# Optimization experiments

Measured on AMD Instinct MI355X. Metric: run time of the kernel, lower is better.

Reference implementation:

```python
import jax, jax.numpy as jnp
import numpy as np

TOPK = 2
ALPHA = 32.0
EPS = 1e-20


def setup_inputs() -> dict:
    key = jax.random.key(0)
    ks = jax.random.split(key, 6)
    E, D, R, Q, V = 16, 2048, 16, 2048, 512
    B, S = 2, 2048
    return {
        "hidden_states": jax.random.normal(ks[0], (B, S, D), jnp.float32),
        "router_weight": jax.random.normal(ks[1], (E, D), jnp.float32) * 0.02,
        "q_lora_a": jax.random.normal(ks[2], (E, D, R), jnp.float32) * 0.02,
        "q_lora_b": jax.random.normal(ks[3], (E, R, Q), jnp.float32) * 0.02,
        "v_lora_a": jax.random.normal(ks[4], (E, D, R), jnp.float32) * 0.02,
        "v_lora_b": jax.random.normal(ks[5], (E, R, V), jnp.float32) * 0.02,
    }


def reference(hidden_states, router_weight, q_lora_a, q_lora_b, v_lora_a, v_lora_b):
    E, D, R = q_lora_a.shape
    Qo = q_lora_b.shape[-1]
    Vo = v_lora_b.shape[-1]
    scale = ALPHA / float(R)
    orig_shape = hidden_states.shape[:-1]
    h = hidden_states.reshape(-1, D)  # [n, D]
    n = h.shape[0]

    # router: top-k softmax probs, renormalized over the k selected experts
    logits = jnp.einsum('nd,ed->ne', h, router_weight)
    probs = jax.nn.softmax(logits, axis=-1)
    scores, idx = jax.lax.top_k(probs, TOPK)          # [n, k]
    scores = scores / (scores.sum(-1, keepdims=True) + EPS)

    # per-token expert combine weights c[n, e] = scale * sum_k score_k * 1[idx_k == e]
    c = jnp.zeros((n, E), h.dtype).at[jnp.arange(n)[:, None], idx].add(scores * scale)

    # dense per-expert low-rank projections; weighting by c makes non-selected
    # experts contribute zero -> identical math to gather + einsum + weighted sum.
    q_low = jnp.einsum('nd,edr->ner', h, q_lora_a) * c[..., None]  # [n, E, R]
    v_low = jnp.einsum('nd,edr->ner', h, v_lora_a) * c[..., None]
    q_delta = jnp.einsum('ner,erq->nq', q_low, q_lora_b)
    v_delta = jnp.einsum('ner,erv->nv', v_low, v_lora_b)

    return (q_delta.reshape(*orig_shape, Qo), v_delta.reshape(*orig_shape, Vo))
```

## Files before the change

### kernel.cpp

```cpp
#include <hip/hip_runtime.h>
#include <math.h>

#define DD 2048
#define EE 16
#define RR 16
#define QO 2048
#define VO 512
#define TILE 128
#define BATCH 16
#define DSPLIT 4
#define DRANGE (DD / DSPLIT)
#define DC 64
#define HSTR (DC + 4)
#define ASTR 20
#define RDC 256
#define T2 32
#define CGQ (QO / 256)
#define CGV (VO / 256)

struct Route { int i0, i1; float w0, w1; };

__global__ __launch_bounds__(256) void router_kernel(
    const float* __restrict__ h, const float* __restrict__ rw,
    Route* __restrict__ route, int n)
{
    __shared__ float  hs[8 * RDC];
    __shared__ double slogd[8 * EE];

    int t0 = blockIdx.x * 8;
    int e  = threadIdx.x >> 4;
    int l  = threadIdx.x & 15;

    double acc[8];
#pragma unroll
    for (int t = 0; t < 8; ++t) acc[t] = 0.0;

    for (int d0 = 0; d0 < DD; d0 += RDC) {
        __syncthreads();
        for (int i = threadIdx.x; i < 8 * (RDC / 4); i += 256) {
            int t = i >> 6, dq = (i & 63) * 4;
            float4 v = make_float4(0.f, 0.f, 0.f, 0.f);
            if (t0 + t < n)
                v = *(const float4*)&h[(size_t)(t0 + t) * DD + d0 + dq];
            *(float4*)&hs[t * RDC + dq] = v;
        }
        __syncthreads();
        const float* rwe = rw + e * DD + d0;
#pragma unroll
        for (int g = 0; g < RDC / 64; ++g) {
            int d = g * 64 + l * 4;
            float4 r4 = *(const float4*)&rwe[d];
            double rx = r4.x, ry = r4.y, rz = r4.z, rw4 = r4.w;
#pragma unroll
            for (int t = 0; t < 8; ++t) {
                float4 hv = *(const float4*)&hs[t * RDC + d];
                acc[t] += (double)hv.x * rx + (double)hv.y * ry
                        + (double)hv.z * rz + (double)hv.w * rw4;
            }
        }
    }
#pragma unroll
    for (int t = 0; t < 8; ++t) {
#pragma unroll
        for (int off = 8; off; off >>= 1)
            acc[t] += __shfl_down(acc[t], off, 16);
    }
    if (l == 0) {
#pragma unroll
        for (int t = 0; t < 8; ++t) slogd[t * EE + e] = acc[t];
    }
    __syncthreads();

    if (threadIdx.x < 8) {
        int t = threadIdx.x, tok = t0 + t;
        if (tok < n) {
            double lg[EE];
#pragma unroll
            for (int i = 0; i < EE; ++i) lg[i] = slogd[t * EE + i];
            int i0 = 0;
            for (int i = 1; i < EE; ++i) if (lg[i] > lg[i0]) i0 = i;
            int i1 = -1;
            for (int i = 0; i < EE; ++i)
                if (i != i0 && (i1 < 0 || lg[i] > lg[i1])) i1 = i;
            double mx = lg[i0], Z = 0.0;
            for (int i = 0; i < EE; ++i) Z += exp(lg[i] - mx);
            double p0 = 1.0 / Z;
            double p1 = exp(lg[i1] - mx) / Z;
            double s  = p0 + p1 + 1e-20;
            Route rt;
            rt.i0 = i0; rt.i1 = i1;
            rt.w0 = (float)(2.0 * p0 / s);
            rt.w1 = (float)(2.0 * p1 / s);
            route[tok] = rt;
        }
    }
}

__global__ __launch_bounds__(256) void a_kernel(
    const float* __restrict__ h, const Route* __restrict__ route,
    const float* __restrict__ qa, const float* __restrict__ va,
    float* __restrict__ low, int n)
{
    int e  = blockIdx.x;
    int t0 = blockIdx.y * TILE;
    int ds = blockIdx.z;

    __shared__ int   sel_tok[TILE];
    __shared__ float sel_w[TILE];
    __shared__ int   sel_k[TILE];
    __shared__ int   sm_cnt;
    if (threadIdx.x == 0) sm_cnt = 0;
    __syncthreads();
    for (int i = threadIdx.x; i < TILE; i += 256) {
        int tok = t0 + i;
        if (tok < n) {
            Route rt = route[tok];
            float w = 0.f; int sel = 0, k = 0;
            if      (rt.i0 == e) { sel = 1; w = rt.w0; k = 0; }
            else if (rt.i1 == e) { sel = 1; w = rt.w1; k = 1; }
            if (sel) {
                int p = atomicAdd(&sm_cnt, 1);
                sel_tok[p] = tok; sel_w[p] = w; sel_k[p] = k;
            }
        }
    }
    __syncthreads();
    int m = sm_cnt;
    if (m == 0) return;

    __align__(16) __shared__ float aq_s[DC * ASTR];
    __align__(16) __shared__ float av_s[DC * ASTR];
    __align__(16) __shared__ float hs[BATCH * HSTR];

    const float* qa_e = qa + (size_t)e * DD * RR;
    const float* va_e = va + (size_t)e * DD * RR;

    int s    = threadIdx.x & 15;
    int tile = threadIdx.x >> 4;
    int tp   = tile >> 2;
    int rp   = tile & 3;

    for (int b0 = 0; b0 < m; b0 += BATCH) {
        int mb = min(BATCH, m - b0);

        float accq[4][4], accv[4][4];
#pragma unroll
        for (int ti = 0; ti < 4; ++ti)
#pragma unroll
            for (int ri = 0; ri < 4; ++ri) { accq[ti][ri] = 0.f; accv[ti][ri] = 0.f; }

        for (int d0 = ds * DRANGE; d0 < (ds + 1) * DRANGE; d0 += DC) {
            __syncthreads();
            {
                int i = threadIdx.x;
                int d = i >> 2, rf = (i & 3) * 4;
                *(float4*)&aq_s[d * ASTR + rf] = *(const float4*)&qa_e[(size_t)(d0 + d) * RR + rf];
                *(float4*)&av_s[d * ASTR + rf] = *(const float4*)&va_e[(size_t)(d0 + d) * RR + rf];
            }
            {
                int i = threadIdx.x;
                int j = i >> 4, dq = (i & 15) * 4;
                float4 v = make_float4(0.f, 0.f, 0.f, 0.f);
                if (j < mb)
                    v = *(const float4*)&h[(size_t)sel_tok[b0 + j] * DD + d0 + dq];
                *(float4*)&hs[j * HSTR + dq] = v;
            }
            __syncthreads();
#pragma unroll
            for (int dd = 0; dd < DC / 16; ++dd) {
                int d = (dd << 4) + s;
                float hv[4];
#pragma unroll
                for (int ti = 0; ti < 4; ++ti)
                    hv[ti] = hs[(tp * 4 + ti) * HSTR + d];
                float4 aqv = *(const float4*)&aq_s[d * ASTR + rp * 4];
                float4 avv = *(const float4*)&av_s[d * ASTR + rp * 4];
                const float* aqp = &aqv.x;
                const float* avp = &avv.x;
#pragma unroll
                for (int ti = 0; ti < 4; ++ti)
#pragma unroll
                    for (int ri = 0; ri < 4; ++ri) {
                        accq[ti][ri] = fmaf(hv[ti], aqp[ri], accq[ti][ri]);
                        accv[ti][ri] = fmaf(hv[ti], avp[ri], accv[ti][ri]);
                    }
            }
        }
#pragma unroll
        for (int ti = 0; ti < 4; ++ti)
#pragma unroll
            for (int ri = 0; ri < 4; ++ri) {
#pragma unroll
                for (int off = 8; off; off >>= 1) {
                    accq[ti][ri] += __shfl_down(accq[ti][ri], off, 16);
                    accv[ti][ri] += __shfl_down(accv[ti][ri], off, 16);
                }
            }
        if (s == 0) {
#pragma unroll
            for (int ti = 0; ti < 4; ++ti) {
                int t = tp * 4 + ti;
                if (t < mb) {
                    int   tok = sel_tok[b0 + t];
                    int   k   = sel_k[b0 + t];
                    float w   = sel_w[b0 + t];
                    size_t base = ((size_t)(tok * 2 + k) * DSPLIT + ds) * 32;
#pragma unroll
                    for (int ri = 0; ri < 4; ++ri) {
                        low[base + rp * 4 + ri]      = accq[ti][ri] * w;
                        low[base + 16 + rp * 4 + ri] = accv[ti][ri] * w;
                    }
                }
            }
        }
        __syncthreads();
    }
}

__global__ __launch_bounds__(256) void b_kernel(
    const Route* __restrict__ route, const float* __restrict__ low,
    const float* __restrict__ qb, const float* __restrict__ vb,
    float* __restrict__ outq, float* __restrict__ outv, int n)
{
    int t0 = blockIdx.x * T2;
    int cg = blockIdx.y;
    int tid = threadIdx.x;

    __shared__ float acc_s[T2 * 256];
    __shared__ float ls[T2 * 2 * RR];
    __shared__ int   elist[EE * T2];
    __shared__ int   ecnt[EE];
    __shared__ Route rts[T2];

    if (tid < EE) ecnt[tid] = 0;
    if (tid < T2) {
        int tok = t0 + tid;
        if (tok < n) rts[tid] = route[tok];
        else { rts[tid].i0 = -1; rts[tid].i1 = -1; rts[tid].w0 = 0.f; rts[tid].w1 = 0.f; }
    }
    __syncthreads();
    if (tid < T2 * 2) {
        int j = tid >> 1, k = tid & 1;
        int e = k ? rts[j].i1 : rts[j].i0;
        if (e >= 0) {
            int p = atomicAdd(&ecnt[e], 1);
            elist[e * T2 + p] = j * 2 + k;
        }
    }
    int side = (cg >= CGQ) ? 1 : 0;
    {
        int slot = tid >> 2, r4 = (tid & 3) * 4;
        int j = slot >> 1, k = slot & 1;
        int tok = t0 + j;
        float4 v = make_float4(0.f, 0.f, 0.f, 0.f);
        if (tok < n) {
            const float* lp = low + (size_t)(tok * 2 + k) * (DSPLIT * 32) + side * 16 + r4;
            float4 p0 = *(const float4*)(lp);
            float4 p1 = *(const float4*)(lp + 32);
            float4 p2 = *(const float4*)(lp + 64);
            float4 p3 = *(const float4*)(lp + 96);
            v.x = p0.x + p1.x + p2.x + p3.x;
            v.y = p0.y + p1.y + p2.y + p3.y;
            v.z = p0.z + p1.z + p2.z + p3.z;
            v.w = p0.w + p1.w + p2.w + p3.w;
        }
        *(float4*)&ls[slot * RR + r4] = v;
    }
#pragma unroll
    for (int j = 0; j < T2; ++j) acc_s[j * 256 + tid] = 0.f;
    __syncthreads();

    const float* bp; float* outp; int W, colbase;
    if (cg < CGQ) { bp = qb; outp = outq; W = QO; colbase = cg * 256; }
    else          { bp = vb; outp = outv; W = VO; colbase = (cg - CGQ) * 256; }
    int col = colbase + tid;

    for (int e = 0; e < EE; ++e) {
        int c = ecnt[e];
        if (c == 0) continue;
        const float* be = bp + (size_t)e * RR * W + col;
        float bc[RR];
#pragma unroll
        for (int r = 0; r < RR; ++r) bc[r] = be[(size_t)r * W];
        for (int ii = 0; ii < c; ++ii) {
            int sk = elist[e * T2 + ii];
            int j  = sk >> 1;
            const float* lp = &ls[sk * RR];
            float4 l0 = *(const float4*)(lp);
            float4 l1 = *(const float4*)(lp + 4);
            float4 l2 = *(const float4*)(lp + 8);
            float4 l3 = *(const float4*)(lp + 12);
            float v = 0.f;
            v = fmaf(l0.x, bc[0],  v); v = fmaf(l0.y, bc[1],  v);
            v = fmaf(l0.z, bc[2],  v); v = fmaf(l0.w, bc[3],  v);
            v = fmaf(l1.x, bc[4],  v); v = fmaf(l1.y, bc[5],  v);
            v = fmaf(l1.z, bc[6],  v); v = fmaf(l1.w, bc[7],  v);
            v = fmaf(l2.x, bc[8],  v); v = fmaf(l2.y, bc[9],  v);
            v = fmaf(l2.z, bc[10], v); v = fmaf(l2.w, bc[11], v);
            v = fmaf(l3.x, bc[12], v); v = fmaf(l3.y, bc[13], v);
            v = fmaf(l3.z, bc[14], v); v = fmaf(l3.w, bc[15], v);
            acc_s[j * 256 + tid] += v;
        }
    }
#pragma unroll
    for (int j = 0; j < T2; ++j) {
        int tok = t0 + j;
        if (tok < n) outp[(size_t)tok * W + col] = acc_s[j * 256 + tid];
    }
}

extern "C" void kernel_launch(void* const* d_in, const int* in_sizes, int n_in,
                              void* d_out, int out_size, void* d_ws, size_t ws_size,
                              hipStream_t stream) {
    const float* h  = (const float*)d_in[0];
    const float* rw = (const float*)d_in[1];
    const float* qa = (const float*)d_in[2];
    const float* qb = (const float*)d_in[3];
    const float* va = (const float*)d_in[4];
    const float* vb = (const float*)d_in[5];

    int n = in_sizes[0] / DD;
    float* out  = (float*)d_out;
    float* outq = out;
    float* outv = out + (size_t)n * QO;

    Route* route = (Route*)d_ws;
    float* low   = (float*)((char*)d_ws + (((size_t)n * 16 + 255) & ~(size_t)255));

    int tiles = (n + TILE - 1) / TILE;

    router_kernel<<<(n + 7) / 8, 256, 0, stream>>>(h, rw, route, n);

    dim3 g2(EE, tiles, DSPLIT);
    a_kernel<<<g2, 256, 0, stream>>>(h, route, qa, va, low, n);

    dim3 g3((n + T2 - 1) / T2, CGQ + CGV);
    b_kernel<<<g3, 256, 0, stream>>>(route, low, qb, vb, outq, outv, n);
}
```

Before: 221.9 us.

## Restructure MoE LoRA kernels: whole-slice A staging, finer D split, prefetched B

The router kernel now handles 4 tokens per block instead of 8, which doubles the number of blocks. The A kernel now stages each expert's whole D-slice of the LoRA A matrices in shared memory once and reuses it across token batches. It splits D eight ways when the workspace is large enough, otherwise four ways with q and v done in two passes. The B kernel builds a compact list of active experts, prefetches the next expert's B columns into registers, and writes outputs as vectorized float4 stores from shared memory. These changes aim to cut repeated A-matrix loads and raise parallelism, at the cost of more shared memory per block, lower occupancy, and more partial sums for the B kernel to reduce.

```diff
diff --git a/kernel.cpp b/kernel.cpp
--- a/kernel.cpp
+++ b/kernel.cpp
@@ -8,15 +8,11 @@
 #define VO 512
 #define TILE 128
 #define BATCH 16
-#define DSPLIT 4
-#define DRANGE (DD / DSPLIT)
-#define DC 64
-#define HSTR (DC + 4)
-#define ASTR 20
+#define T2 32
+#define CGQ 8
+#define CGV 2
+#define RTB 4
 #define RDC 256
-#define T2 32
-#define CGQ (QO / 256)
-#define CGV (VO / 256)
 
 struct Route { int i0, i1; float w0, w1; };
 
@@ -24,21 +20,19 @@
     const float* __restrict__ h, const float* __restrict__ rw,
     Route* __restrict__ route, int n)
 {
-    __shared__ float  hs[8 * RDC];
-    __shared__ double slogd[8 * EE];
-
-    int t0 = blockIdx.x * 8;
+    __shared__ float  hs[RTB * RDC];
+    __shared__ double slogd[RTB * EE];
+
+    int t0 = blockIdx.x * RTB;
     int e  = threadIdx.x >> 4;
     int l  = threadIdx.x & 15;
 
-    double acc[8];
-#pragma unroll
-    for (int t = 0; t < 8; ++t) acc[t] = 0.0;
+    double acc[RTB] = {0.0, 0.0, 0.0, 0.0};
 
     for (int d0 = 0; d0 < DD; d0 += RDC) {
         __syncthreads();
-        for (int i = threadIdx.x; i < 8 * (RDC / 4); i += 256) {
-            int t = i >> 6, dq = (i & 63) * 4;
+        {
+            int t = threadIdx.x >> 6, dq = (threadIdx.x & 63) * 4;
             float4 v = make_float4(0.f, 0.f, 0.f, 0.f);
             if (t0 + t < n)
                 v = *(const float4*)&h[(size_t)(t0 + t) * DD + d0 + dq];
@@ -52,7 +46,7 @@
             float4 r4 = *(const float4*)&rwe[d];
             double rx = r4.x, ry = r4.y, rz = r4.z, rw4 = r4.w;
 #pragma unroll
-            for (int t = 0; t < 8; ++t) {
+            for (int t = 0; t < RTB; ++t) {
                 float4 hv = *(const float4*)&hs[t * RDC + d];
                 acc[t] += (double)hv.x * rx + (double)hv.y * ry
                         + (double)hv.z * rz + (double)hv.w * rw4;
@@ -60,18 +54,18 @@
         }
     }
 #pragma unroll
-    for (int t = 0; t < 8; ++t) {
+    for (int t = 0; t < RTB; ++t) {
 #pragma unroll
         for (int off = 8; off; off >>= 1)
             acc[t] += __shfl_down(acc[t], off, 16);
     }
     if (l == 0) {
 #pragma unroll
-        for (int t = 0; t < 8; ++t) slogd[t * EE + e] = acc[t];
-    }
-    __syncthreads();
-
-    if (threadIdx.x < 8) {
+        for (int t = 0; t < RTB; ++t) slogd[t * EE + e] = acc[t];
+    }
+    __syncthreads();
+
+    if (threadIdx.x < RTB) {
         int t = threadIdx.x, tok = t0 + t;
         if (tok < n) {
             double lg[EE];
@@ -96,11 +90,13 @@
     }
 }
 
+template<int DSPLIT, bool TWOPASS>
 __global__ __launch_bounds__(256) void a_kernel(
     const float* __restrict__ h, const Route* __restrict__ route,
     const float* __restrict__ qa, const float* __restrict__ va,
     float* __restrict__ low, int n)
 {
+    constexpr int DR = DD / DSPLIT;
     int e  = blockIdx.x;
     int t0 = blockIdx.y * TILE;
     int ds = blockIdx.z;
@@ -115,12 +111,12 @@
         int tok = t0 + i;
         if (tok < n) {
             Route rt = route[tok];
-            float w = 0.f; int sel = 0, k = 0;
-            if      (rt.i0 == e) { sel = 1; w = rt.w0; k = 0; }
-            else if (rt.i1 == e) { sel = 1; w = rt.w1; k = 1; }
-            if (sel) {
+            if (rt.i0 == e) {
                 int p = atomicAdd(&sm_cnt, 1);
-                sel_tok[p] = tok; sel_w[p] = w; sel_k[p] = k;
+                sel_tok[p] = tok; sel_w[p] = rt.w0; sel_k[p] = 0;
+            } else if (rt.i1 == e) {
+                int p = atomicAdd(&sm_cnt, 1);
+                sel_tok[p] = tok; sel_w[p] = rt.w1; sel_k[p] = 1;
             }
         }
     }
@@ -128,95 +124,145 @@
     int m = sm_cnt;
     if (m == 0) return;
 
-    __align__(16) __shared__ float aq_s[DC * ASTR];
-    __align__(16) __shared__ float av_s[DC * ASTR];
-    __align__(16) __shared__ float hs[BATCH * HSTR];
-
-    const float* qa_e = qa + (size_t)e * DD * RR;
-    const float* va_e = va + (size_t)e * DD * RR;
+    __align__(16) __shared__ float a_s[(TWOPASS ? 1 : 2) * DR * RR];
+    __align__(16) __shared__ float hs[BATCH * DR];
+
+    const float* aq_e = qa + (size_t)e * DD * RR + (size_t)ds * DR * RR;
+    const float* av_e = va + (size_t)e * DD * RR + (size_t)ds * DR * RR;
 
     int s    = threadIdx.x & 15;
     int tile = threadIdx.x >> 4;
     int tp   = tile >> 2;
     int rp   = tile & 3;
 
-    for (int b0 = 0; b0 < m; b0 += BATCH) {
-        int mb = min(BATCH, m - b0);
-
-        float accq[4][4], accv[4][4];
-#pragma unroll
-        for (int ti = 0; ti < 4; ++ti)
-#pragma unroll
-            for (int ri = 0; ri < 4; ++ri) { accq[ti][ri] = 0.f; accv[ti][ri] = 0.f; }
-
-        for (int d0 = ds * DRANGE; d0 < (ds + 1) * DRANGE; d0 += DC) {
+    constexpr int NMAT = TWOPASS ? 2 : 1;
+    for (int mat = 0; mat < NMAT; ++mat) {
+        __syncthreads();
+        if (TWOPASS) {
+            const float* ap = mat ? av_e : aq_e;
+            for (int t = threadIdx.x; t < DR * RR / 4; t += 256) {
+                int d = t >> 2, rf = (t & 3) * 4;
+                *(float4*)&a_s[d * RR + rf] = *(const float4*)&ap[(size_t)d * RR + rf];
+            }
+        } else {
+            for (int t = threadIdx.x; t < 2 * DR * RR / 4; t += 256) {
+                int which = t >= DR * RR / 4;
+                int tt = which ? t - DR * RR / 4 : t;
+                int d = tt >> 2, rf = (tt & 3) * 4;
+                const float* ap = which ? av_e : aq_e;
+                *(float4*)&a_s[which * DR * RR + d * RR + rf] =
+                    *(const float4*)&ap[(size_t)d * RR + rf];
+            }
+        }
+
+        for (int b0 = 0; b0 < m; b0 += BATCH) {
+            int mb = min(BATCH, m - b0);
             __syncthreads();
-            {
-                int i = threadIdx.x;
-                int d = i >> 2, rf = (i & 3) * 4;
-                *(float4*)&aq_s[d * ASTR + rf] = *(const float4*)&qa_e[(size_t)(d0 + d) * RR + rf];
-                *(float4*)&av_s[d * ASTR + rf] = *(const float4*)&va_e[(size_t)(d0 + d) * RR + rf];
-            }
-            {
-                int i = threadIdx.x;
-                int j = i >> 4, dq = (i & 15) * 4;
+            for (int t = threadIdx.x; t < BATCH * DR / 4; t += 256) {
+                int j = t / (DR / 4), f = (t % (DR / 4)) * 4;
                 float4 v = make_float4(0.f, 0.f, 0.f, 0.f);
                 if (j < mb)
-                    v = *(const float4*)&h[(size_t)sel_tok[b0 + j] * DD + d0 + dq];
-                *(float4*)&hs[j * HSTR + dq] = v;
+                    v = *(const float4*)&h[(size_t)sel_tok[b0 + j] * DD + ds * DR + f];
+                *(float4*)&hs[j * DR + f] = v;
             }
             __syncthreads();
-#pragma unroll
-            for (int dd = 0; dd < DC / 16; ++dd) {
-                int d = (dd << 4) + s;
-                float hv[4];
+
+            if (!TWOPASS) {
+                float accq[4][4] = {}, accv[4][4] = {};
+#pragma unroll
+                for (int dd = 0; dd < DR / 16; ++dd) {
+                    int d = dd * 16 + s;
+                    float4 a0 = *(const float4*)&a_s[d * RR + rp * 4];
+                    float4 a1 = *(const float4*)&a_s[DR * RR + d * RR + rp * 4];
+                    float hv[4];
+#pragma unroll
+                    for (int ti = 0; ti < 4; ++ti)
+                        hv[ti] = hs[(tp * 4 + ti) * DR + d];
+                    const float* q4 = &a0.x;
+                    const float* v4 = &a1.x;
+#pragma unroll
+                    for (int ti = 0; ti < 4; ++ti)
+#pragma unroll
+                        for (int ri = 0; ri < 4; ++ri) {
+                            accq[ti][ri] = fmaf(hv[ti], q4[ri], accq[ti][ri]);
+                            accv[ti][ri] = fmaf(hv[ti], v4[ri], accv[ti][ri]);
+                        }
+                }
 #pragma unroll
                 for (int ti = 0; ti < 4; ++ti)
-                    hv[ti] = hs[(tp * 4 + ti) * HSTR + d];
-                float4 aqv = *(const float4*)&aq_s[d * ASTR + rp * 4];
-                float4 avv = *(const float4*)&av_s[d * ASTR + rp * 4];
-                const float* aqp = &aqv.x;
-                const float* avp = &avv.x;
-#pragma unroll
-                for (int ti = 0; ti < 4; ++ti)
 #pragma unroll
                     for (int ri = 0; ri < 4; ++ri) {
-                        accq[ti][ri] = fmaf(hv[ti], aqp[ri], accq[ti][ri]);
-                        accv[ti][ri] = fmaf(hv[ti], avp[ri], accv[ti][ri]);
+#pragma unroll
+                        for (int off = 8; off; off >>= 1) {
+                            accq[ti][ri] += __shfl_down(accq[ti][ri], off, 16);
+                            accv[ti][ri] += __shfl_down(accv[ti][ri], off, 16);
+                        }
                     }
-            }
-        }
-#pragma unroll
-        for (int ti = 0; ti < 4; ++ti)
-#pragma unroll
-            for (int ri = 0; ri < 4; ++ri) {
-#pragma unroll
-                for (int off = 8; off; off >>= 1) {
-                    accq[ti][ri] += __shfl_down(accq[ti][ri], off, 16);
-                    accv[ti][ri] += __shfl_down(accv[ti][ri], off, 16);
-                }
-            }
-        if (s == 0) {
-#pragma unroll
-            for (int ti = 0; ti < 4; ++ti) {
-                int t = tp * 4 + ti;
-                if (t < mb) {
-                    int   tok = sel_tok[b0 + t];
-                    int   k   = sel_k[b0 + t];
-                    float w   = sel_w[b0 + t];
-                    size_t base = ((size_t)(tok * 2 + k) * DSPLIT + ds) * 32;
-#pragma unroll
-                    for (int ri = 0; ri < 4; ++ri) {
-                        low[base + rp * 4 + ri]      = accq[ti][ri] * w;
-                        low[base + 16 + rp * 4 + ri] = accv[ti][ri] * w;
+                if (s == 0) {
+#pragma unroll
+                    for (int ti = 0; ti < 4; ++ti) {
+                        int t = tp * 4 + ti;
+                        if (t < mb) {
+                            int   tok = sel_tok[b0 + t];
+                            int   k   = sel_k[b0 + t];
+                            float w   = sel_w[b0 + t];
+                            float* dst = low + ((size_t)(tok * 2 + k) * DSPLIT + ds) * 32;
+                            float4 vq = make_float4(accq[ti][0]*w, accq[ti][1]*w,
+                                                    accq[ti][2]*w, accq[ti][3]*w);
+                            float4 vv = make_float4(accv[ti][0]*w, accv[ti][1]*w,
+                                                    accv[ti][2]*w, accv[ti][3]*w);
+                            *(float4*)&dst[rp * 4]      = vq;
+                            *(float4*)&dst[16 + rp * 4] = vv;
+                        }
                     }
                 }
-            }
-        }
-        __syncthreads();
+            } else {
+                float acc[4][4] = {};
+#pragma unroll
+                for (int dd = 0; dd < DR / 16; ++dd) {
+                    int d = dd * 16 + s;
+                    float4 a0 = *(const float4*)&a_s[d * RR + rp * 4];
+                    float hv[4];
+#pragma unroll
+                    for (int ti = 0; ti < 4; ++ti)
+                        hv[ti] = hs[(tp * 4 + ti) * DR + d];
+                    const float* q4 = &a0.x;
+#pragma unroll
+                    for (int ti = 0; ti < 4; ++ti)
+#pragma unroll
+                        for (int ri = 0; ri < 4; ++ri)
+                            acc[ti][ri] = fmaf(hv[ti], q4[ri], acc[ti][ri]);
+                }
+#pragma unroll
+                for (int ti = 0; ti < 4; ++ti)
+#pragma unroll
+                    for (int ri = 0; ri < 4; ++ri) {
+#pragma unroll
+                        for (int off = 8; off; off >>= 1)
+                            acc[ti][ri] += __shfl_down(acc[ti][ri], off, 16);
+                    }
+                if (s == 0) {
+#pragma unroll
+                    for (int ti = 0; ti < 4; ++ti) {
+                        int t = tp * 4 + ti;
+                        if (t < mb) {
+                            int   tok = sel_tok[b0 + t];
+                            int   k   = sel_k[b0 + t];
+                            float w   = sel_w[b0 + t];
+                            float* dst = low + ((size_t)(tok * 2 + k) * DSPLIT + ds) * 32
+                                       + mat * 16;
+                            float4 vq = make_float4(acc[ti][0]*w, acc[ti][1]*w,
+                                                    acc[ti][2]*w, acc[ti][3]*w);
+                            *(float4*)&dst[rp * 4] = vq;
+                        }
+                    }
+                }
+            }
+        }
     }
 }
 
+template<int DSPLIT>
 __global__ __launch_bounds__(256) void b_kernel(
     const Route* __restrict__ route, const float* __restrict__ low,
     const float* __restrict__ qb, const float* __restrict__ vb,
@@ -230,13 +276,17 @@
     __shared__ float ls[T2 * 2 * RR];
     __shared__ int   elist[EE * T2];
     __shared__ int   ecnt[EE];
+    __shared__ int   plist[EE];
+    __shared__ int   pcnt;
     __shared__ Route rts[T2];
 
     if (tid < EE) ecnt[tid] = 0;
+    if (tid == 0) pcnt = 0;
     if (tid < T2) {
         int tok = t0 + tid;
-        if (tok < n) rts[tid] = route[tok];
-        else { rts[tid].i0 = -1; rts[tid].i1 = -1; rts[tid].w0 = 0.f; rts[tid].w1 = 0.f; }
+        Route rt; rt.i0 = -1; rt.i1 = -1; rt.w0 = 0.f; rt.w1 = 0.f;
+        if (tok < n) rt = route[tok];
+        rts[tid] = rt;
     }
     __syncthreads();
     if (tid < T2 * 2) {
@@ -250,62 +300,79 @@
     int side = (cg >= CGQ) ? 1 : 0;
     {
         int slot = tid >> 2, r4 = (tid & 3) * 4;
-        int j = slot >> 1, k = slot & 1;
-        int tok = t0 + j;
+        int j = slot >> 1;
         float4 v = make_float4(0.f, 0.f, 0.f, 0.f);
-        if (tok < n) {
-            const float* lp = low + (size_t)(tok * 2 + k) * (DSPLIT * 32) + side * 16 + r4;
-            float4 p0 = *(const float4*)(lp);
-            float4 p1 = *(const float4*)(lp + 32);
-            float4 p2 = *(const float4*)(lp + 64);
-            float4 p3 = *(const float4*)(lp + 96);
-            v.x = p0.x + p1.x + p2.x + p3.x;
-            v.y = p0.y + p1.y + p2.y + p3.y;
-            v.z = p0.z + p1.z + p2.z + p3.z;
-            v.w = p0.w + p1.w + p2.w + p3.w;
+        if (t0 + j < n) {
+            const float* lp = low + (size_t)((t0 + j) * 2 + (slot & 1)) * (DSPLIT * 32)
+                            + side * 16 + r4;
+#pragma unroll
+            for (int p = 0; p < DSPLIT; ++p) {
+                float4 q = *(const float4*)(lp + p * 32);
+                v.x += q.x; v.y += q.y; v.z += q.z; v.w += q.w;
+            }
         }
         *(float4*)&ls[slot * RR + r4] = v;
     }
 #pragma unroll
     for (int j = 0; j < T2; ++j) acc_s[j * 256 + tid] = 0.f;
     __syncthreads();
+    if (tid < EE && ecnt[tid] > 0) { int p = atomicAdd(&pcnt, 1); plist[p] = tid; }
+    __syncthreads();
+    int P = pcnt;
 
     const float* bp; float* outp; int W, colbase;
     if (cg < CGQ) { bp = qb; outp = outq; W = QO; colbase = cg * 256; }
     else          { bp = vb; outp = outv; W = VO; colbase = (cg - CGQ) * 256; }
     int col = colbase + tid;
 
-    for (int e = 0; e < EE; ++e) {
-        int c = ecnt[e];
-        if (c == 0) continue;
-        const float* be = bp + (size_t)e * RR * W + col;
+    if (P > 0) {
         float bc[RR];
-#pragma unroll
-        for (int r = 0; r < RR; ++r) bc[r] = be[(size_t)r * W];
-        for (int ii = 0; ii < c; ++ii) {
-            int sk = elist[e * T2 + ii];
-            int j  = sk >> 1;
-            const float* lp = &ls[sk * RR];
-            float4 l0 = *(const float4*)(lp);
-            float4 l1 = *(const float4*)(lp + 4);
-            float4 l2 = *(const float4*)(lp + 8);
-            float4 l3 = *(const float4*)(lp + 12);
-            float v = 0.f;
-            v = fmaf(l0.x, bc[0],  v); v = fmaf(l0.y, bc[1],  v);
-            v = fmaf(l0.z, bc[2],  v); v = fmaf(l0.w, bc[3],  v);
-            v = fmaf(l1.x, bc[4],  v); v = fmaf(l1.y, bc[5],  v);
-            v = fmaf(l1.z, bc[6],  v); v = fmaf(l1.w, bc[7],  v);
-            v = fmaf(l2.x, bc[8],  v); v = fmaf(l2.y, bc[9],  v);
-            v = fmaf(l2.z, bc[10], v); v = fmaf(l2.w, bc[11], v);
-            v = fmaf(l3.x, bc[12], v); v = fmaf(l3.y, bc[13], v);
-            v = fmaf(l3.z, bc[14], v); v = fmaf(l3.w, bc[15], v);
-            acc_s[j * 256 + tid] += v;
-        }
-    }
-#pragma unroll
-    for (int j = 0; j < T2; ++j) {
+        {
+            const float* be = bp + (size_t)plist[0] * RR * W + col;
+#pragma unroll
+            for (int r = 0; r < RR; ++r) bc[r] = be[(size_t)r * W];
+        }
+        for (int p = 0; p < P; ++p) {
+            float bn[RR];
+            if (p + 1 < P) {
+                const float* be = bp + (size_t)plist[p + 1] * RR * W + col;
+#pragma unroll
+                for (int r = 0; r < RR; ++r) bn[r] = be[(size_t)r * W];
+            }
+            int e = plist[p], c = ecnt[e];
+            for (int ii = 0; ii < c; ++ii) {
+                int sk = elist[e * T2 + ii];
+                int j  = sk >> 1;
+                const float* lp = &ls[sk * RR];
+                float4 l0 = *(const float4*)(lp);
+                float4 l1 = *(const float4*)(lp + 4);
+                float4 l2 = *(const float4*)(lp + 8);
+                float4 l3 = *(const float4*)(lp + 12);
+                float v = 0.f;
+                v = fmaf(l0.x, bc[0],  v); v = fmaf(l0.y, bc[1],  v);
+                v = fmaf(l0.z, bc[2],  v); v = fmaf(l0.w, bc[3],  v);
+                v = fmaf(l1.x, bc[4],  v); v = fmaf(l1.y, bc[5],  v);
+                v = fmaf(l1.z, bc[6],  v); v = fmaf(l1.w, bc[7],  v);
+                v = fmaf(l2.x, bc[8],  v); v = fmaf(l2.y, bc[9],  v);
+                v = fmaf(l2.z, bc[10], v); v = fmaf(l2.w, bc[11], v);
+                v = fmaf(l3.x, bc[12], v); v = fmaf(l3.y, bc[13], v);
+                v = fmaf(l3.z, bc[14], v); v = fmaf(l3.w, bc[15], v);
+                acc_s[j * 256 + tid] += v;
+            }
+            if (p + 1 < P) {
+#pragma unroll
+                for (int r = 0; r < RR; ++r) bc[r] = bn[r];
+            }
+        }
+    }
+    __syncthreads();
+    for (int t = tid; t < T2 * 64; t += 256) {
+        int j = t >> 6, fq = (t & 63) * 4;
         int tok = t0 + j;
-        if (tok < n) outp[(size_t)tok * W + col] = acc_s[j * 256 + tid];
+        if (tok < n) {
+            float4 v = *(const float4*)&acc_s[j * 256 + fq];
+            *(float4*)&outp[(size_t)tok * W + colbase + fq] = v;
+        }
     }
 }
 
@@ -324,16 +391,22 @@
     float* outq = out;
     float* outv = out + (size_t)n * QO;
 
+    size_t route_b = ((size_t)n * 16 + 255) & ~(size_t)255;
     Route* route = (Route*)d_ws;
-    float* low   = (float*)((char*)d_ws + (((size_t)n * 16 + 255) & ~(size_t)255));
+    float* low   = (float*)((char*)d_ws + route_b);
+    size_t need8 = route_b + (size_t)n * 2 * 8 * 32 * 4;
 
     int tiles = (n + TILE - 1) / TILE;
-
-    router_kernel<<<(n + 7) / 8, 256, 0, stream>>>(h, rw, route, n);
-
-    dim3 g2(EE, tiles, DSPLIT);
-    a_kernel<<<g2, 256, 0, stream>>>(h, route, qa, va, low, n);
+    router_kernel<<<(n + RTB - 1) / RTB, 256, 0, stream>>>(h, rw, route, n);
 
     dim3 g3((n + T2 - 1) / T2, CGQ + CGV);
-    b_kernel<<<g3, 256, 0, stream>>>(route, low, qb, vb, outq, outv, n);
+    if (ws_size >= need8) {
+        dim3 g2(EE, tiles, 8);
+        a_kernel<8, false><<<g2, 256, 0, stream>>>(h, route, qa, va, low, n);
+        b_kernel<8><<<g3, 256, 0, stream>>>(route, low, qb, vb, outq, outv, n);
+    } else {
+        dim3 g2(EE, tiles, 4);
+        a_kernel<4, true><<<g2, 256, 0, stream>>>(h, route, qa, va, low, n);
+        b_kernel<4><<<g3, 256, 0, stream>>>(route, low, qb, vb, outq, outv, n);
+    }
 }
```

After: 239.5 us. +7.9%, slower.

## Use bf16 MFMA for expert A-projection with global expert lists and wave-per-token router

Applied to the files above, without the earlier changes.

Replaces the FP32 FMA A-projection with a bf16 MFMA kernel that works on per-expert token lists built by the router through global atomics. A prep kernel converts and transposes the LoRA-A weights to bf16, and the router now gives one wave per token using shuffles. The B kernel gains register prefetch of the next expert's weights and vectorized output stores. This cuts the wasted per-tile scanning and the scalar FMA cost, in exchange for bf16 rounding of activations and weights, nondeterministic list order, and an extra memset and prep launch.

```diff
diff --git a/kernel.cpp b/kernel.cpp
--- a/kernel.cpp
+++ b/kernel.cpp
@@ -1,4 +1,5 @@
 #include <hip/hip_runtime.h>
+#include <hip/hip_bf16.h>
 #include <math.h>
 
 #define DD 2048
@@ -6,214 +7,181 @@
 #define RR 16
 #define QO 2048
 #define VO 512
-#define TILE 128
-#define BATCH 16
-#define DSPLIT 4
-#define DRANGE (DD / DSPLIT)
-#define DC 64
-#define HSTR (DC + 4)
-#define ASTR 20
-#define RDC 256
+#define KS 4
+#define KRANGE (DD / KS)
+#define KC 256
+#define MT 32
+#define HS 264
 #define T2 32
-#define CGQ (QO / 256)
-#define CGV (VO / 256)
+#define CGQ 8
+#define CGV 2
+
+typedef __attribute__((ext_vector_type(8))) short bf16x8;
+typedef __attribute__((ext_vector_type(4))) float f32x4;
 
 struct Route { int i0, i1; float w0, w1; };
+
+__device__ inline unsigned short f2bf(float x) {
+    __hip_bfloat16 b = __float2bfloat16(x);
+    return *reinterpret_cast<unsigned short*>(&b);
+}
+
+__global__ __launch_bounds__(256) void prep_ab_kernel(
+    const float* __restrict__ qa, const float* __restrict__ va,
+    unsigned short* __restrict__ abT)
+{
+    int e  = blockIdx.x;
+    int dq = blockIdx.y;
+    __align__(16) __shared__ unsigned short t_s[32 * 128];
+    int tid = threadIdx.x;
+    for (int d0 = dq * 512; d0 < dq * 512 + 512; d0 += 128) {
+        __syncthreads();
+#pragma unroll
+        for (int it = 0; it < 8; ++it) {
+            int idx = tid + it * 256;
+            int dd = idx >> 4, r = idx & 15;
+            float q = qa[((size_t)e * DD + d0 + dd) * RR + r];
+            float v = va[((size_t)e * DD + d0 + dd) * RR + r];
+            t_s[r * 128 + dd]        = f2bf(q);
+            t_s[(16 + r) * 128 + dd] = f2bf(v);
+        }
+        __syncthreads();
+#pragma unroll
+        for (int it = 0; it < 2; ++it) {
+            int idx = tid + it * 256;
+            int row = idx >> 4, c8 = (idx & 15) * 8;
+            uint4 v = *(const uint4*)&t_s[row * 128 + c8];
+            *(uint4*)&abT[((size_t)e * 32 + row) * DD + d0 + c8] = v;
+        }
+    }
+}
 
 __global__ __launch_bounds__(256) void router_kernel(
     const float* __restrict__ h, const float* __restrict__ rw,
-    Route* __restrict__ route, int n)
+    Route* __restrict__ route, int* __restrict__ cnt,
+    int* __restrict__ elist, float* __restrict__ wlist, int n)
 {
-    __shared__ float  hs[8 * RDC];
-    __shared__ double slogd[8 * EE];
-
-    int t0 = blockIdx.x * 8;
-    int e  = threadIdx.x >> 4;
-    int l  = threadIdx.x & 15;
-
-    double acc[8];
-#pragma unroll
-    for (int t = 0; t < 8; ++t) acc[t] = 0.0;
-
-    for (int d0 = 0; d0 < DD; d0 += RDC) {
-        __syncthreads();
-        for (int i = threadIdx.x; i < 8 * (RDC / 4); i += 256) {
-            int t = i >> 6, dq = (i & 63) * 4;
-            float4 v = make_float4(0.f, 0.f, 0.f, 0.f);
-            if (t0 + t < n)
-                v = *(const float4*)&h[(size_t)(t0 + t) * DD + d0 + dq];
-            *(float4*)&hs[t * RDC + dq] = v;
-        }
-        __syncthreads();
-        const float* rwe = rw + e * DD + d0;
-#pragma unroll
-        for (int g = 0; g < RDC / 64; ++g) {
-            int d = g * 64 + l * 4;
-            float4 r4 = *(const float4*)&rwe[d];
-            double rx = r4.x, ry = r4.y, rz = r4.z, rw4 = r4.w;
-#pragma unroll
-            for (int t = 0; t < 8; ++t) {
-                float4 hv = *(const float4*)&hs[t * RDC + d];
-                acc[t] += (double)hv.x * rx + (double)hv.y * ry
-                        + (double)hv.z * rz + (double)hv.w * rw4;
-            }
-        }
-    }
-#pragma unroll
-    for (int t = 0; t < 8; ++t) {
-#pragma unroll
-        for (int off = 8; off; off >>= 1)
-            acc[t] += __shfl_down(acc[t], off, 16);
-    }
-    if (l == 0) {
-#pragma unroll
-        for (int t = 0; t < 8; ++t) slogd[t * EE + e] = acc[t];
-    }
-    __syncthreads();
-
-    if (threadIdx.x < 8) {
-        int t = threadIdx.x, tok = t0 + t;
-        if (tok < n) {
-            double lg[EE];
-#pragma unroll
-            for (int i = 0; i < EE; ++i) lg[i] = slogd[t * EE + i];
-            int i0 = 0;
-            for (int i = 1; i < EE; ++i) if (lg[i] > lg[i0]) i0 = i;
-            int i1 = -1;
-            for (int i = 0; i < EE; ++i)
-                if (i != i0 && (i1 < 0 || lg[i] > lg[i1])) i1 = i;
-            double mx = lg[i0], Z = 0.0;
-            for (int i = 0; i < EE; ++i) Z += exp(lg[i] - mx);
-            double p0 = 1.0 / Z;
-            double p1 = exp(lg[i1] - mx) / Z;
-            double s  = p0 + p1 + 1e-20;
-            Route rt;
-            rt.i0 = i0; rt.i1 = i1;
-            rt.w0 = (float)(2.0 * p0 / s);
-            rt.w1 = (float)(2.0 * p1 / s);
-            route[tok] = rt;
-        }
-    }
-}
-
-__global__ __launch_bounds__(256) void a_kernel(
-    const float* __restrict__ h, const Route* __restrict__ route,
-    const float* __restrict__ qa, const float* __restrict__ va,
-    float* __restrict__ low, int n)
+    int wave = threadIdx.x >> 6;
+    int lane = threadIdx.x & 63;
+    int tok  = blockIdx.x * 4 + wave;
+    if (tok >= n) return;
+    int e = lane >> 2, ds = lane & 3;
+    const float* hp = h + (size_t)tok * DD;
+    const float* rp = rw + (size_t)e * DD;
+    double acc0 = 0.0, acc1 = 0.0;
+    for (int i = 0; i < 64; ++i) {
+        int d0 = i * 16 + ds * 4;
+        int d1 = d0 + 1024;
+        float4 h0 = *(const float4*)&hp[d0];
+        float4 r0 = *(const float4*)&rp[d0];
+        float4 h1 = *(const float4*)&hp[d1];
+        float4 r1 = *(const float4*)&rp[d1];
+        acc0 += (double)h0.x * r0.x + (double)h0.y * r0.y
+              + (double)h0.z * r0.z + (double)h0.w * r0.w;
+        acc1 += (double)h1.x * r1.x + (double)h1.y * r1.y
+              + (double)h1.z * r1.z + (double)h1.w * r1.w;
+    }
+    double acc = acc0 + acc1;
+    acc += __shfl_xor(acc, 1, 64);
+    acc += __shfl_xor(acc, 2, 64);
+    double lg[EE];
+#pragma unroll
+    for (int i = 0; i < EE; ++i) lg[i] = __shfl(acc, i * 4, 64);
+    int i0 = 0;
+    for (int i = 1; i < EE; ++i) if (lg[i] > lg[i0]) i0 = i;
+    int i1 = -1;
+    for (int i = 0; i < EE; ++i)
+        if (i != i0 && (i1 < 0 || lg[i] > lg[i1])) i1 = i;
+    if (lane == 0) {
+        double mx = lg[i0], Z = 0.0;
+        for (int i = 0; i < EE; ++i) Z += exp(lg[i] - mx);
+        double p0 = 1.0 / Z;
+        double p1 = exp(lg[i1] - mx) / Z;
+        double s  = p0 + p1 + 1e-20;
+        float w0 = (float)(2.0 * p0 / s);
+        float w1 = (float)(2.0 * p1 / s);
+        Route rt; rt.i0 = i0; rt.i1 = i1; rt.w0 = w0; rt.w1 = w1;
+        route[tok] = rt;
+        int p0i = atomicAdd(&cnt[i0], 1);
+        elist[(size_t)i0 * n + p0i] = tok * 2 + 0;
+        wlist[(size_t)i0 * n + p0i] = w0;
+        int p1i = atomicAdd(&cnt[i1], 1);
+        elist[(size_t)i1 * n + p1i] = tok * 2 + 1;
+        wlist[(size_t)i1 * n + p1i] = w1;
+    }
+}
+
+__global__ __launch_bounds__(256) void a_mfma_kernel(
+    const float* __restrict__ h, const unsigned short* __restrict__ abT,
+    const int* __restrict__ cnt, const int* __restrict__ elist,
+    const float* __restrict__ wlist, float* __restrict__ low, int n)
 {
     int e  = blockIdx.x;
-    int t0 = blockIdx.y * TILE;
-    int ds = blockIdx.z;
-
-    __shared__ int   sel_tok[TILE];
-    __shared__ float sel_w[TILE];
-    __shared__ int   sel_k[TILE];
-    __shared__ int   sm_cnt;
-    if (threadIdx.x == 0) sm_cnt = 0;
-    __syncthreads();
-    for (int i = threadIdx.x; i < TILE; i += 256) {
-        int tok = t0 + i;
-        if (tok < n) {
-            Route rt = route[tok];
-            float w = 0.f; int sel = 0, k = 0;
-            if      (rt.i0 == e) { sel = 1; w = rt.w0; k = 0; }
-            else if (rt.i1 == e) { sel = 1; w = rt.w1; k = 1; }
-            if (sel) {
-                int p = atomicAdd(&sm_cnt, 1);
-                sel_tok[p] = tok; sel_w[p] = w; sel_k[p] = k;
-            }
-        }
-    }
-    __syncthreads();
-    int m = sm_cnt;
-    if (m == 0) return;
-
-    __align__(16) __shared__ float aq_s[DC * ASTR];
-    __align__(16) __shared__ float av_s[DC * ASTR];
-    __align__(16) __shared__ float hs[BATCH * HSTR];
-
-    const float* qa_e = qa + (size_t)e * DD * RR;
-    const float* va_e = va + (size_t)e * DD * RR;
-
-    int s    = threadIdx.x & 15;
-    int tile = threadIdx.x >> 4;
-    int tp   = tile >> 2;
-    int rp   = tile & 3;
-
-    for (int b0 = 0; b0 < m; b0 += BATCH) {
-        int mb = min(BATCH, m - b0);
-
-        float accq[4][4], accv[4][4];
-#pragma unroll
-        for (int ti = 0; ti < 4; ++ti)
-#pragma unroll
-            for (int ri = 0; ri < 4; ++ri) { accq[ti][ri] = 0.f; accv[ti][ri] = 0.f; }
-
-        for (int d0 = ds * DRANGE; d0 < (ds + 1) * DRANGE; d0 += DC) {
+    int ks = blockIdx.z;
+    int me = cnt[e];
+
+    __align__(16) __shared__ unsigned short hb_s[MT * HS];
+    __align__(16) __shared__ unsigned short ab_s[MT * HS];
+    __shared__ int   sel_e[MT];
+    __shared__ float sel_w[MT];
+
+    int tid  = threadIdx.x;
+    int lane = tid & 63, wave = tid >> 6;
+    int mhalf = wave >> 1, nhalf = wave & 1;
+    int l15 = lane & 15, quad = lane >> 4;
+
+    for (int tile = blockIdx.y; tile * MT < me; tile += gridDim.y) {
+        __syncthreads();
+        if (tid < MT) {
+            int sl = tile * MT + tid;
+            int entry = 0; float w = 0.f;
+            if (sl < me) {
+                entry = elist[(size_t)e * n + sl];
+                w     = wlist[(size_t)e * n + sl];
+            }
+            sel_e[tid] = entry; sel_w[tid] = w;
+        }
+        __syncthreads();
+
+        f32x4 acc = {0.f, 0.f, 0.f, 0.f};
+        for (int c = 0; c < KRANGE / KC; ++c) {
+            int kbase = ks * KRANGE + c * KC;
+            if (c) __syncthreads();
+#pragma unroll
+            for (int it = 0; it < 8; ++it) {
+                int idx = tid + it * 256;
+                int row = idx >> 6, c4 = (idx & 63) * 4;
+                int tokk = sel_e[row] >> 1;
+                float4 v = *(const float4*)&h[(size_t)tokk * DD + kbase + c4];
+                ushort4 b;
+                b.x = f2bf(v.x); b.y = f2bf(v.y); b.z = f2bf(v.z); b.w = f2bf(v.w);
+                *(ushort4*)&hb_s[row * HS + c4] = b;
+            }
+#pragma unroll
+            for (int it = 0; it < 4; ++it) {
+                int idx = tid + it * 256;
+                int row = idx >> 5, c8 = (idx & 31) * 8;
+                uint4 v = *(const uint4*)&abT[((size_t)e * 32 + row) * DD + kbase + c8];
+                *(uint4*)&ab_s[row * HS + c8] = v;
+            }
             __syncthreads();
-            {
-                int i = threadIdx.x;
-                int d = i >> 2, rf = (i & 3) * 4;
-                *(float4*)&aq_s[d * ASTR + rf] = *(const float4*)&qa_e[(size_t)(d0 + d) * RR + rf];
-                *(float4*)&av_s[d * ASTR + rf] = *(const float4*)&va_e[(size_t)(d0 + d) * RR + rf];
-            }
-            {
-                int i = threadIdx.x;
-                int j = i >> 4, dq = (i & 15) * 4;
-                float4 v = make_float4(0.f, 0.f, 0.f, 0.f);
-                if (j < mb)
-                    v = *(const float4*)&h[(size_t)sel_tok[b0 + j] * DD + d0 + dq];
-                *(float4*)&hs[j * HSTR + dq] = v;
-            }
-            __syncthreads();
-#pragma unroll
-            for (int dd = 0; dd < DC / 16; ++dd) {
-                int d = (dd << 4) + s;
-                float hv[4];
-#pragma unroll
-                for (int ti = 0; ti < 4; ++ti)
-                    hv[ti] = hs[(tp * 4 + ti) * HSTR + d];
-                float4 aqv = *(const float4*)&aq_s[d * ASTR + rp * 4];
-                float4 avv = *(const float4*)&av_s[d * ASTR + rp * 4];
-                const float* aqp = &aqv.x;
-                const float* avp = &avv.x;
-#pragma unroll
-                for (int ti = 0; ti < 4; ++ti)
-#pragma unroll
-                    for (int ri = 0; ri < 4; ++ri) {
-                        accq[ti][ri] = fmaf(hv[ti], aqp[ri], accq[ti][ri]);
-                        accv[ti][ri] = fmaf(hv[ti], avp[ri], accv[ti][ri]);
-                    }
-            }
-        }
-#pragma unroll
-        for (int ti = 0; ti < 4; ++ti)
-#pragma unroll
-            for (int ri = 0; ri < 4; ++ri) {
-#pragma unroll
-                for (int off = 8; off; off >>= 1) {
-                    accq[ti][ri] += __shfl_down(accq[ti][ri], off, 16);
-                    accv[ti][ri] += __shfl_down(accv[ti][ri], off, 16);
-                }
-            }
-        if (s == 0) {
-#pragma unroll
-            for (int ti = 0; ti < 4; ++ti) {
-                int t = tp * 4 + ti;
-                if (t < mb) {
-                    int   tok = sel_tok[b0 + t];
-                    int   k   = sel_k[b0 + t];
-                    float w   = sel_w[b0 + t];
-                    size_t base = ((size_t)(tok * 2 + k) * DSPLIT + ds) * 32;
-#pragma unroll
-                    for (int ri = 0; ri < 4; ++ri) {
-                        low[base + rp * 4 + ri]      = accq[ti][ri] * w;
-                        low[base + 16 + rp * 4 + ri] = accv[ti][ri] * w;
-                    }
-                }
-            }
-        }
-        __syncthreads();
+#pragma unroll
+            for (int s = 0; s < KC / 32; ++s) {
+                bf16x8 af = *(const bf16x8*)&hb_s[(mhalf * 16 + l15) * HS + s * 32 + quad * 8];
+                bf16x8 bf = *(const bf16x8*)&ab_s[(nhalf * 16 + l15) * HS + s * 32 + quad * 8];
+                acc = __builtin_amdgcn_mfma_f32_16x16x32_bf16(af, bf, acc, 0, 0, 0);
+            }
+        }
+#pragma unroll
+        for (int r = 0; r < 4; ++r) {
+            int mrow = quad * 4 + r;
+            int sl = tile * MT + mhalf * 16 + mrow;
+            if (sl < me) {
+                int   entry = sel_e[mhalf * 16 + mrow];
+                float w     = sel_w[mhalf * 16 + mrow];
+                low[(size_t)entry * (KS * 32) + ks * 32 + nhalf * 16 + l15] = acc[r] * w;
+            }
+        }
     }
 }
 
@@ -228,15 +196,19 @@
 
     __shared__ float acc_s[T2 * 256];
     __shared__ float ls[T2 * 2 * RR];
-    __shared__ int   elist[EE * T2];
+    __shared__ int   elist_s[EE * T2];
     __shared__ int   ecnt[EE];
+    __shared__ int   plist[EE];
+    __shared__ int   pcnt;
     __shared__ Route rts[T2];
 
     if (tid < EE) ecnt[tid] = 0;
+    if (tid == 0) pcnt = 0;
     if (tid < T2) {
         int tok = t0 + tid;
-        if (tok < n) rts[tid] = route[tok];
-        else { rts[tid].i0 = -1; rts[tid].i1 = -1; rts[tid].w0 = 0.f; rts[tid].w1 = 0.f; }
+        Route rt; rt.i0 = -1; rt.i1 = -1; rt.w0 = 0.f; rt.w1 = 0.f;
+        if (tok < n) rt = route[tok];
+        rts[tid] = rt;
     }
     __syncthreads();
     if (tid < T2 * 2) {
@@ -244,68 +216,85 @@
         int e = k ? rts[j].i1 : rts[j].i0;
         if (e >= 0) {
             int p = atomicAdd(&ecnt[e], 1);
-            elist[e * T2 + p] = j * 2 + k;
+            elist_s[e * T2 + p] = j * 2 + k;
         }
     }
     int side = (cg >= CGQ) ? 1 : 0;
     {
         int slot = tid >> 2, r4 = (tid & 3) * 4;
-        int j = slot >> 1, k = slot & 1;
-        int tok = t0 + j;
+        int j = slot >> 1;
         float4 v = make_float4(0.f, 0.f, 0.f, 0.f);
-        if (tok < n) {
-            const float* lp = low + (size_t)(tok * 2 + k) * (DSPLIT * 32) + side * 16 + r4;
-            float4 p0 = *(const float4*)(lp);
-            float4 p1 = *(const float4*)(lp + 32);
-            float4 p2 = *(const float4*)(lp + 64);
-            float4 p3 = *(const float4*)(lp + 96);
-            v.x = p0.x + p1.x + p2.x + p3.x;
-            v.y = p0.y + p1.y + p2.y + p3.y;
-            v.z = p0.z + p1.z + p2.z + p3.z;
-            v.w = p0.w + p1.w + p2.w + p3.w;
+        if (t0 + j < n) {
+            const float* lp = low + (size_t)((t0 + j) * 2 + (slot & 1)) * (KS * 32)
+                            + side * 16 + r4;
+#pragma unroll
+            for (int p = 0; p < KS; ++p) {
+                float4 q = *(const float4*)(lp + p * 32);
+                v.x += q.x; v.y += q.y; v.z += q.z; v.w += q.w;
+            }
         }
         *(float4*)&ls[slot * RR + r4] = v;
     }
 #pragma unroll
     for (int j = 0; j < T2; ++j) acc_s[j * 256 + tid] = 0.f;
     __syncthreads();
+    if (tid < EE && ecnt[tid] > 0) { int p = atomicAdd(&pcnt, 1); plist[p] = tid; }
+    __syncthreads();
+    int P = pcnt;
 
     const float* bp; float* outp; int W, colbase;
     if (cg < CGQ) { bp = qb; outp = outq; W = QO; colbase = cg * 256; }
     else          { bp = vb; outp = outv; W = VO; colbase = (cg - CGQ) * 256; }
     int col = colbase + tid;
 
-    for (int e = 0; e < EE; ++e) {
-        int c = ecnt[e];
-        if (c == 0) continue;
-        const float* be = bp + (size_t)e * RR * W + col;
+    if (P > 0) {
         float bc[RR];
-#pragma unroll
-        for (int r = 0; r < RR; ++r) bc[r] = be[(size_t)r * W];
-        for (int ii = 0; ii < c; ++ii) {
-            int sk = elist[e * T2 + ii];
-            int j  = sk >> 1;
-            const float* lp = &ls[sk * RR];
-            float4 l0 = *(const float4*)(lp);
-            float4 l1 = *(const float4*)(lp + 4);
-            float4 l2 = *(const float4*)(lp + 8);
-            float4 l3 = *(const float4*)(lp + 12);
-            float v = 0.f;
-            v = fmaf(l0.x, bc[0],  v); v = fmaf(l0.y, bc[1],  v);
-            v = fmaf(l0.z, bc[2],  v); v = fmaf(l0.w, bc[3],  v);
-            v = fmaf(l1.x, bc[4],  v); v = fmaf(l1.y, bc[5],  v);
-            v = fmaf(l1.z, bc[6],  v); v = fmaf(l1.w, bc[7],  v);
-            v = fmaf(l2.x, bc[8],  v); v = fmaf(l2.y, bc[9],  v);
-            v = fmaf(l2.z, bc[10], v); v = fmaf(l2.w, bc[11], v);
-            v = fmaf(l3.x, bc[12], v); v = fmaf(l3.y, bc[13], v);
-            v = fmaf(l3.z, bc[14], v); v = fmaf(l3.w, bc[15], v);
-            acc_s[j * 256 + tid] += v;
-        }
-    }
-#pragma unroll
-    for (int j = 0; j < T2; ++j) {
+        {
+            const float* be = bp + (size_t)plist[0] * RR * W + col;
+#pragma unroll
+            for (int r = 0; r < RR; ++r) bc[r] = be[(size_t)r * W];
+        }
+        for (int p = 0; p < P; ++p) {
+            float bn[RR];
+            if (p + 1 < P) {
+                const float* be = bp + (size_t)plist[p + 1] * RR * W + col;
+#pragma unroll
+                for (int r = 0; r < RR; ++r) bn[r] = be[(size_t)r * W];
+            }
+            int e = plist[p], c = ecnt[e];
+            for (int ii = 0; ii < c; ++ii) {
+                int sk = elist_s[e * T2 + ii];
+                int j  = sk >> 1;
+                const float* lp = &ls[sk * RR];
+                float4 l0 = *(const float4*)(lp);
+                float4 l1 = *(const float4*)(lp + 4);
+                float4 l2 = *(const float4*)(lp + 8);
+                float4 l3 = *(const float4*)(lp + 12);
+                float v = 0.f;
+                v = fmaf(l0.x, bc[0],  v); v = fmaf(l0.y, bc[1],  v);
+                v = fmaf(l0.z, bc[2],  v); v = fmaf(l0.w, bc[3],  v);
+                v = fmaf(l1.x, bc[4],  v); v = fmaf(l1.y, bc[5],  v);
+                v = fmaf(l1.z, bc[6],  v); v = fmaf(l1.w, bc[7],  v);
+                v = fmaf(l2.x, bc[8],  v); v = fmaf(l2.y, bc[9],  v);
+                v = fmaf(l2.z, bc[10], v); v = fmaf(l2.w, bc[11], v);
+                v = fmaf(l3.x, bc[12], v); v = fmaf(l3.y, bc[13], v);
+                v = fmaf(l3.z, bc[14], v); v = fmaf(l3.w, bc[15], v);
+                acc_s[j * 256 + tid] += v;
+            }
+            if (p + 1 < P) {
+#pragma unroll
+                for (int r = 0; r < RR; ++r) bc[r] = bn[r];
+            }
+        }
+    }
+    __syncthreads();
+    for (int t = tid; t < T2 * 64; t += 256) {
+        int j = t >> 6, fq = (t & 63) * 4;
         int tok = t0 + j;
-        if (tok < n) outp[(size_t)tok * W + col] = acc_s[j * 256 + tid];
+        if (tok < n) {
+            float4 v = *(const float4*)&acc_s[j * 256 + fq];
+            *(float4*)&outp[(size_t)tok * W + colbase + fq] = v;
+        }
     }
 }
 
@@ -324,15 +313,25 @@
     float* outq = out;
     float* outv = out + (size_t)n * QO;
 
-    Route* route = (Route*)d_ws;
-    float* low   = (float*)((char*)d_ws + (((size_t)n * 16 + 255) & ~(size_t)255));
-
-    int tiles = (n + TILE - 1) / TILE;
-
-    router_kernel<<<(n + 7) / 8, 256, 0, stream>>>(h, rw, route, n);
-
-    dim3 g2(EE, tiles, DSPLIT);
-    a_kernel<<<g2, 256, 0, stream>>>(h, route, qa, va, low, n);
+    char* w = (char*)d_ws;
+    auto align256 = [](size_t x) { return (x + 255) & ~(size_t)255; };
+    Route* route = (Route*)w;                       size_t off = align256((size_t)n * sizeof(Route));
+    int*   cnt   = (int*)(w + off);                 off = align256(off + EE * sizeof(int));
+    int*   elist = (int*)(w + off);                 off = align256(off + (size_t)EE * n * sizeof(int));
+    float* wlist = (float*)(w + off);               off = align256(off + (size_t)EE * n * sizeof(float));
+    unsigned short* abT = (unsigned short*)(w + off); off = align256(off + (size_t)EE * 32 * DD * sizeof(unsigned short));
+    float* low   = (float*)(w + off);
+
+    dim3 g0(EE, 4);
+    prep_ab_kernel<<<g0, 256, 0, stream>>>(qa, va, abT);
+
+    hipMemsetAsync(cnt, 0, EE * sizeof(int), stream);
+
+    router_kernel<<<(n + 3) / 4, 256, 0, stream>>>(h, rw, route, cnt, elist, wlist, n);
+
+    int ytiles = (2 * n / EE + MT - 1) / MT + 4;
+    dim3 g2(EE, ytiles, KS);
+    a_mfma_kernel<<<g2, 256, 0, stream>>>(h, abT, cnt, elist, wlist, low, n);
 
     dim3 g3((n + T2 - 1) / T2, CGQ + CGV);
     b_kernel<<<g3, 256, 0, stream>>>(route, low, qb, vb, outq, outv, n);
```

Result: slower. 289.4 us (+30.4%).
